# Kernel tuning notes

Measured on AMD Instinct MI355X. Metric: run time of the kernel, lower is better.

The kernel has to match this reference:

```python
import jax, jax.numpy as jnp
from jax import lax
import numpy as np

BN_EPS = 1e-3

def _hard_sigmoid(x):
    # Keras hard_sigmoid: relu6(x + 3) / 6
    return jnp.clip(x / 6.0 + 0.5, 0.0, 1.0)

def _conv(x, w):
    # x: [B,H,W,C], w: [kh,kw,C,Cout]
    return lax.conv_general_dilated(x, w, window_strides=(1, 1), padding='SAME',
                                    dimension_numbers=('NHWC', 'HWIO', 'NHWC'))

def _convlstm(x, Wx, Wh, b):
    # x: [B,T,H,W,C] -> [B,T,H,W,F]; gates packed i,f,c,o along last dim (Keras order)
    B, T, H, W, C = x.shape
    F = b.shape[0] // 4
    h0 = jnp.zeros((B, H, W, F), x.dtype)
    c0 = jnp.zeros_like(h0)

    def step(carry, xt):
        h, c = carry
        z = _conv(xt, Wx) + _conv(h, Wh) + b  # [B,H,W,4F]
        i, f, g, o = jnp.split(z, 4, axis=-1)
        c = _hard_sigmoid(f) * c + _hard_sigmoid(i) * jnp.tanh(g)
        h = _hard_sigmoid(o) * jnp.tanh(c)
        return (h, c), h

    _, hs = lax.scan(step, (h0, c0), jnp.moveaxis(x, 1, 0))  # [T,B,H,W,F]
    return jnp.moveaxis(hs, 0, 1)


def setup_inputs() -> dict:
    key = jax.random.key(0)
    ks = jax.random.split(key, 8)
    B, T, H, W, C, F = 4, 16, 64, 64, 48, 48
    x = jax.random.normal(ks[0], (B, T, H, W, C), jnp.float32)
    s = 0.05  # keep gate pre-activations in a sane range
    Wx1 = jax.random.normal(ks[1], (3, 3, C, 4 * F), jnp.float32) * s
    Wh1 = jax.random.normal(ks[2], (3, 3, F, 4 * F), jnp.float32) * s
    b1 = jax.random.normal(ks[3], (4 * F,), jnp.float32) * s
    Wx2 = jax.random.normal(ks[4], (3, 3, F, 4 * F), jnp.float32) * s
    Wh2 = jax.random.normal(ks[5], (3, 3, F, 4 * F), jnp.float32) * s
    b2 = jax.random.normal(ks[6], (4 * F,), jnp.float32) * s
    gamma = jnp.ones((F,), jnp.float32)
    beta = jnp.zeros((F,), jnp.float32)
    mean = jax.random.normal(ks[7], (F,), jnp.float32) * 0.1
    var = jax.random.uniform(jax.random.fold_in(key, 99), (F,), jnp.float32, 0.5, 1.5)
    return {"x": x, "Wx1": Wx1, "Wh1": Wh1, "b1": b1,
            "Wx2": Wx2, "Wh2": Wh2, "b2": b2,
            "gamma": gamma, "beta": beta, "mean": mean, "var": var}


def reference(x, Wx1, Wh1, b1, Wx2, Wh2, b2, gamma, beta, mean, var):
    h = _convlstm(x, Wx1, Wh1, b1)
    # Dropout(0.2) at inference: identity. BatchNorm (inference, per-channel):
    h = gamma * (h - mean) * lax.rsqrt(var + BN_EPS) + beta
    h = _convlstm(h, Wx2, Wh2, b2)
    return x + h  # channels match (C == filters) -> direct residual add
```

## Files before the change

### kernel.cpp

```cpp
#include <hip/hip_runtime.h>
#include <hip/hip_bf16.h>

typedef __bf16 bf16;
typedef __bf16 bf16x8 __attribute__((ext_vector_type(8)));
typedef float  f32x4  __attribute__((ext_vector_type(4)));
typedef unsigned short u16x8 __attribute__((ext_vector_type(8)));

#define NB 4
#define NT 16
#define NH 64
#define NW 64
#define NC 48
#define RSTR 104
#define RKY  (66*RSTR)

__device__ __forceinline__ float hsig(float x){
    return fminf(fmaxf(x*0.16666667f + 0.5f, 0.0f), 1.0f);
}
__device__ __forceinline__ float ftanh(float x){
    float ax = fabsf(x);
    float e  = __expf(-2.0f*ax);
    float r  = (1.0f - e) * __builtin_amdgcn_rcpf(1.0f + e);
    return __builtin_copysignf(r, x);
}

__global__ void detect_dtype(const unsigned* __restrict__ g, int* __restrict__ flag){
    if (threadIdx.x == 0 && blockIdx.x == 0)
        *flag = (g[0] == 0x3F803F80u) ? 1 : 0;
}

__device__ __forceinline__ float ld_any(const void* p, int i, int isbf){
    return isbf ? (float)((const bf16*)p)[i] : ((const float*)p)[i];
}

__global__ void prep_weights(const void* __restrict__ Wx, const void* __restrict__ Wh,
                             const int* __restrict__ flag, bf16* __restrict__ Wsw){
    int isbf = *flag;
    int idx = blockIdx.x*256 + threadIdx.x;
    if (idx >= 165888) return;
    int e    = idx & 7;
    int lane = (idx >> 3) & 63;
    int nt   = (idx >> 9) % 12;
    int krk  = idx / (512*12);
    int ky = krk / 9, kr = krk % 9;
    int ln = lane & 15, lg = lane >> 4;
    int n_new  = nt*16 + ln;
    int gate = n_new & 3, c = n_new >> 2;
    int n_orig = gate*48 + c;
    int k  = kr*32 + lg*8 + e;
    int kx = k / 96, ch = k % 96;
    float v = (ch < 48) ? ld_any(Wx, ((ky*3+kx)*48 + ch)*192 + n_orig, isbf)
                        : ld_any(Wh, ((ky*3+kx)*48 + (ch-48))*192 + n_orig, isbf);
    Wsw[idx] = (bf16)v;
}

__global__ void prep_params(const void* b1, const void* b2, const void* gamma,
                            const void* beta, const void* mean, const void* var,
                            const int* __restrict__ flag, float* __restrict__ P){
    int isbf = *flag;
    int i = blockIdx.x*64 + threadIdx.x;
    if (i < 192)      P[i] = ld_any(b1, i, isbf);
    else if (i < 384) P[i] = ld_any(b2, i-192, isbf);
    else if (i < 432){
        int c = i-384;
        P[i] = ld_any(gamma,c,isbf) * rsqrtf(ld_any(var,c,isbf) + 1e-3f);
    } else if (i < 480){
        int c = i-432;
        float sc = ld_any(gamma,c,isbf) * rsqrtf(ld_any(var,c,isbf) + 1e-3f);
        P[i] = ld_any(beta,c,isbf) - ld_any(mean,c,isbf)*sc;
    }
}

template<int LAYER>
__global__ __launch_bounds__(256, 1)
void step_kernel(const void* __restrict__ xseq,
                 const bf16* __restrict__ hin,
                 bf16*       __restrict__ hout,
                 float*      __restrict__ cbuf,
                 const bf16* __restrict__ Wsw,
                 const float* __restrict__ P,
                 const void* __restrict__ xres,
                 bf16*       __restrict__ seqout,
                 void*       __restrict__ outp,
                 const int* __restrict__ flag,
                 int t)
{
    __shared__ bf16  rowpad[3*RKY];
    __shared__ float zbuf[64*196];
    const int isbf = *flag;
    const int tid = threadIdx.x;
    const int img = blockIdx.x >> 6;
    const int y   = blockIdx.x & 63;

    if (tid < 78){
        int ky = tid/26; int rmd = tid%26;
        int col = (rmd < 13) ? 0 : 65; int q = rmd % 13;
        u16x8 z = {};
        *(u16x8*)(rowpad + ky*RKY + col*RSTR + q*8) = z;
    }
    for (int task = tid; task < 2304; task += 256){
        int part = task / 384;
        int chn  = task % 384;
        int ky = part >> 1, half = part & 1;
        int row = y + ky - 1;
        int xcol = chn / 6;
        int c0   = (chn % 6)*8;
        u16x8 val = {};
        if (row >= 0 && row < NH){
            if (half == 1){
                val = *(const u16x8*)(hin + ((img*NH + row)*NW + xcol)*NC + c0);
            } else {
                int si = (((img*NT + t)*NH + row)*NW + xcol)*NC + c0;
                if (LAYER == 2 || isbf){
                    val = *(const u16x8*)((const bf16*)xseq + si);
                } else {
                    const float* src = (const float*)xseq + si;
                    bf16x8 v;
                    #pragma unroll
                    for (int u = 0; u < 8; ++u) v[u] = (bf16)src[u];
                    val = *(u16x8*)&v;
                }
            }
        }
        *(u16x8*)(rowpad + ky*RKY + (xcol+1)*RSTR + half*48 + c0) = val;
    }
    __syncthreads();

    const int lane = tid & 63;
    const int wv   = tid >> 6;
    const int ln   = lane & 15;
    const int lg   = lane >> 4;

    f32x4 acc[4][3] = {};

    #pragma unroll
    for (int ky = 0; ky < 3; ++ky){
        #pragma unroll 3
        for (int kr = 0; kr < 9; ++kr){
            const bf16* wp = Wsw + (size_t)((ky*9 + kr)*12 + wv*3)*512 + lane*8;
            bf16x8 b0 = *(const bf16x8*)(wp);
            bf16x8 b1 = *(const bf16x8*)(wp + 512);
            bf16x8 b2 = *(const bf16x8*)(wp + 1024);
            const bf16* ap = rowpad + ky*RKY + (ln + (kr/3))*RSTR + (kr%3)*32 + lg*8;
            #pragma unroll
            for (int mt = 0; mt < 4; ++mt){
                bf16x8 a = *(const bf16x8*)(ap + mt*16*RSTR);
                acc[mt][0] = __builtin_amdgcn_mfma_f32_16x16x32_bf16(a, b0, acc[mt][0], 0,0,0);
                acc[mt][1] = __builtin_amdgcn_mfma_f32_16x16x32_bf16(a, b1, acc[mt][1], 0,0,0);
                acc[mt][2] = __builtin_amdgcn_mfma_f32_16x16x32_bf16(a, b2, acc[mt][2], 0,0,0);
            }
        }
    }

    #pragma unroll
    for (int mt = 0; mt < 4; ++mt)
        #pragma unroll
        for (int j = 0; j < 3; ++j)
            #pragma unroll
            for (int r = 0; r < 4; ++r)
                zbuf[(mt*16 + lg*4 + r)*196 + wv*48 + j*16 + ln] = acc[mt][j][r];
    __syncthreads();

    const float* Pb = P + (LAYER == 1 ? 0 : 192);
    #pragma unroll 4
    for (int it = 0; it < 12; ++it){
        int cell = tid + it*256;
        int pos  = cell / 48;
        int c    = cell - pos*48;
        f32x4 z = *(const f32x4*)(zbuf + pos*196 + c*4);
        float zi = z[0] + Pb[c];
        float zf = z[1] + Pb[48+c];
        float zg = z[2] + Pb[96+c];
        float zo = z[3] + Pb[144+c];
        int gi = ((img*NH + y)*NW + pos)*NC + c;
        float cold = cbuf[gi];
        float cn = hsig(zf)*cold + hsig(zi)*ftanh(zg);
        float hn = hsig(zo)*ftanh(cn);
        cbuf[gi] = cn;
        hout[gi] = (bf16)hn;
        int sidx = (((img*NT + t)*NH + y)*NW + pos)*NC + c;
        if (LAYER == 1){
            seqout[sidx] = (bf16)(hn*P[384+c] + P[432+c]);
        } else {
            float xr = isbf ? (float)((const bf16*)xres)[sidx]
                            : ((const float*)xres)[sidx];
            float v = xr + hn;
            if (isbf) ((bf16*)outp)[sidx] = (bf16)v;
            else      ((float*)outp)[sidx] = v;
        }
    }
}

extern "C" void kernel_launch(void* const* d_in, const int* in_sizes, int n_in,
                              void* d_out, int out_size, void* d_ws, size_t ws_size,
                              hipStream_t stream)
{
    const void* x     = d_in[0];
    const void* Wx1   = d_in[1];
    const void* Wh1   = d_in[2];
    const void* b1    = d_in[3];
    const void* Wx2   = d_in[4];
    const void* Wh2   = d_in[5];
    const void* b2    = d_in[6];
    const void* gamma = d_in[7];
    const void* beta  = d_in[8];
    const void* mean  = d_in[9];
    const void* var   = d_in[10];

    char* p = (char*)d_ws;
    auto carve = [&](size_t bytes)->void*{
        void* q = (void*)p; p += (bytes + 255) & ~(size_t)255; return q;
    };
    const size_t planeN = (size_t)NB*NH*NW*NC;
    int*   flag = (int*)  carve(256);
    float* P    = (float*)carve(480*sizeof(float));
    bf16*  Wc1  = (bf16*) carve(165888*sizeof(bf16));
    bf16*  Wc2  = (bf16*) carve(165888*sizeof(bf16));
    bf16*  hA   = (bf16*) carve(planeN*sizeof(bf16));
    bf16*  hB   = (bf16*) carve(planeN*sizeof(bf16));
    float* cb   = (float*)carve(planeN*sizeof(float));
    bf16*  seq  = (bf16*) carve((size_t)NB*NT*NH*NW*NC*sizeof(bf16));

    detect_dtype<<<1, 64, 0, stream>>>((const unsigned*)gamma, flag);

    prep_weights<<<648, 256, 0, stream>>>(Wx1, Wh1, flag, Wc1);
    prep_weights<<<648, 256, 0, stream>>>(Wx2, Wh2, flag, Wc2);
    prep_params<<<8, 64, 0, stream>>>(b1, b2, gamma, beta, mean, var, flag, P);

    hipMemsetAsync(hA, 0, planeN*sizeof(bf16),  stream);
    hipMemsetAsync(cb, 0, planeN*sizeof(float), stream);
    bf16 *hr = hA, *hw = hB;
    for (int t = 0; t < NT; ++t){
        step_kernel<1><<<NB*NH, 256, 0, stream>>>(x, hr, hw, cb, Wc1, P,
                                                  nullptr, seq, nullptr, flag, t);
        bf16* tmp = hr; hr = hw; hw = tmp;
    }
    hipMemsetAsync(hr, 0, planeN*sizeof(bf16),  stream);
    hipMemsetAsync(cb, 0, planeN*sizeof(float), stream);
    for (int t = 0; t < NT; ++t){
        step_kernel<2><<<NB*NH, 256, 0, stream>>>(seq, hr, hw, cb, Wc2, P,
                                                  x, nullptr, d_out, flag, t);
        bf16* tmp = hr; hr = hw; hw = tmp;
    }
}
```

Measured before the change: 685.1 us.

## Fuse all ConvLSTM timesteps and both layers into one persistent kernel

Replaces the 32 per-timestep launches with a single persistent kernel of 256 blocks, one per (image, row). Blocks synchronise through per-row progress flags, each waiting only on its two neighbouring rows, using release stores and spin-waits. The cell state stays in registers instead of a global buffer, and the block's own new h row goes straight into LDS. The next timestep's input rows are staged while the gates are computed, so launch overhead, the global cell-state traffic and memsets go away. The trade-off is that correctness depends on all blocks being resident at once (otherwise the spin-waits deadlock), and the cross-block flag protocol carries subtle race risks.

```diff
diff --git a/kernel.cpp b/kernel.cpp
--- a/kernel.cpp
+++ b/kernel.cpp
@@ -71,26 +71,33 @@
     }
 }
 
-template<int LAYER>
 __global__ __launch_bounds__(256, 1)
-void step_kernel(const void* __restrict__ xseq,
-                 const bf16* __restrict__ hin,
-                 bf16*       __restrict__ hout,
-                 float*      __restrict__ cbuf,
-                 const bf16* __restrict__ Wsw,
-                 const float* __restrict__ P,
-                 const void* __restrict__ xres,
-                 bf16*       __restrict__ seqout,
-                 void*       __restrict__ outp,
-                 const int* __restrict__ flag,
-                 int t)
+void fused_kernel(const void* __restrict__ x,
+                  bf16* __restrict__ seq,
+                  bf16* __restrict__ hA,
+                  bf16* __restrict__ hB,
+                  const bf16* __restrict__ Wc1,
+                  const bf16* __restrict__ Wc2,
+                  const float* __restrict__ P,
+                  void* __restrict__ outp,
+                  const int* __restrict__ flag,
+                  int* __restrict__ done)
 {
     __shared__ bf16  rowpad[3*RKY];
     __shared__ float zbuf[64*196];
     const int isbf = *flag;
-    const int tid = threadIdx.x;
-    const int img = blockIdx.x >> 6;
-    const int y   = blockIdx.x & 63;
+    const int tid  = threadIdx.x;
+    const int xcd  = blockIdx.x & 7;
+    const int slot = blockIdx.x >> 3;
+    const int img  = xcd >> 1;
+    const int y    = ((xcd & 1) << 5) | slot;
+    const int lane = tid & 63;
+    const int wv   = tid >> 6;
+    const int ln   = lane & 15;
+    const int lg   = lane >> 4;
+
+    int* dme  = done + img*NH + y;
+    int* dimg = done + img*NH;
 
     if (tid < 78){
         int ky = tid/26; int rmd = tid%26;
@@ -98,95 +105,150 @@
         u16x8 z = {};
         *(u16x8*)(rowpad + ky*RKY + col*RSTR + q*8) = z;
     }
-    for (int task = tid; task < 2304; task += 256){
-        int part = task / 384;
-        int chn  = task % 384;
-        int ky = part >> 1, half = part & 1;
-        int row = y + ky - 1;
-        int xcol = chn / 6;
-        int c0   = (chn % 6)*8;
-        u16x8 val = {};
-        if (row >= 0 && row < NH){
-            if (half == 1){
-                val = *(const u16x8*)(hin + ((img*NH + row)*NW + xcol)*NC + c0);
-            } else {
-                int si = (((img*NT + t)*NH + row)*NW + xcol)*NC + c0;
-                if (LAYER == 2 || isbf){
-                    val = *(const u16x8*)((const bf16*)xseq + si);
+
+    float creg[12];
+
+    #pragma unroll
+    for (int L = 0; L < 2; ++L){
+        const bf16*  Wsw = L ? Wc2 : Wc1;
+        const float* Pb  = P + (L ? 192 : 0);
+        const void*  xs  = L ? (const void*)seq : x;
+        const int    xbf = L ? 1 : isbf;
+
+        float bi_[3], bf_[3], bg_[3], bo_[3], bns[3], bnb[3];
+        #pragma unroll
+        for (int q = 0; q < 3; ++q){
+            int cq = (tid + q*16) % 48;
+            bi_[q] = Pb[cq];      bf_[q] = Pb[48+cq];
+            bg_[q] = Pb[96+cq];   bo_[q] = Pb[144+cq];
+            bns[q] = P[384+cq];   bnb[q] = P[432+cq];
+        }
+
+        auto stage_x = [&](int tt){
+            for (int task = tid; task < 1152; task += 256){
+                int ky = task/384, chn = task%384;
+                int xcol = chn/6, c0 = (chn%6)*8;
+                int row = y + ky - 1;
+                u16x8 val = {};
+                if (row >= 0 && row < NH){
+                    int si = (((img*NT + tt)*NH + row)*NW + xcol)*NC + c0;
+                    if (xbf){
+                        val = *(const u16x8*)((const bf16*)xs + si);
+                    } else {
+                        const float* src = (const float*)xs + si;
+                        bf16x8 v;
+                        #pragma unroll
+                        for (int u = 0; u < 8; ++u) v[u] = (bf16)src[u];
+                        val = *(u16x8*)&v;
+                    }
+                }
+                *(u16x8*)(rowpad + ky*RKY + (xcol+1)*RSTR + c0) = val;
+            }
+        };
+
+        stage_x(0);
+        for (int task = tid; task < 1152; task += 256){
+            int ky = task/384, chn = task%384;
+            int xcol = chn/6, c0 = (chn%6)*8;
+            u16x8 z = {};
+            *(u16x8*)(rowpad + ky*RKY + (xcol+1)*RSTR + 48 + c0) = z;
+        }
+        #pragma unroll
+        for (int i = 0; i < 12; ++i) creg[i] = 0.f;
+        __syncthreads();
+
+        #pragma unroll 1
+        for (int t = 0; t < NT; ++t){
+            bf16* hw = ((t + L) & 1) ? hB : hA;
+
+            f32x4 acc[4][3] = {};
+            #pragma unroll
+            for (int ky = 0; ky < 3; ++ky){
+                #pragma unroll 3
+                for (int kr = 0; kr < 9; ++kr){
+                    const bf16* wp = Wsw + (size_t)((ky*9 + kr)*12 + wv*3)*512 + lane*8;
+                    bf16x8 b0 = *(const bf16x8*)(wp);
+                    bf16x8 b1 = *(const bf16x8*)(wp + 512);
+                    bf16x8 b2 = *(const bf16x8*)(wp + 1024);
+                    const bf16* ap = rowpad + ky*RKY + (ln + (kr/3))*RSTR + (kr%3)*32 + lg*8;
+                    #pragma unroll
+                    for (int mt = 0; mt < 4; ++mt){
+                        bf16x8 a = *(const bf16x8*)(ap + mt*16*RSTR);
+                        acc[mt][0] = __builtin_amdgcn_mfma_f32_16x16x32_bf16(a, b0, acc[mt][0], 0,0,0);
+                        acc[mt][1] = __builtin_amdgcn_mfma_f32_16x16x32_bf16(a, b1, acc[mt][1], 0,0,0);
+                        acc[mt][2] = __builtin_amdgcn_mfma_f32_16x16x32_bf16(a, b2, acc[mt][2], 0,0,0);
+                    }
+                }
+            }
+
+            #pragma unroll
+            for (int mt = 0; mt < 4; ++mt)
+                #pragma unroll
+                for (int j = 0; j < 3; ++j)
+                    #pragma unroll
+                    for (int r = 0; r < 4; ++r)
+                        zbuf[(mt*16 + lg*4 + r)*196 + wv*48 + j*16 + ln] = acc[mt][j][r];
+            __syncthreads();
+
+            if (t < NT-1) stage_x(t+1);
+
+            #pragma unroll
+            for (int it = 0; it < 12; ++it){
+                const int q = it % 3;
+                int cell = tid + it*256;
+                int pos = cell/48;
+                int c = cell - pos*48;
+                f32x4 z = *(const f32x4*)(zbuf + pos*196 + c*4);
+                float cn = hsig(z[1]+bf_[q])*creg[it] + hsig(z[0]+bi_[q])*ftanh(z[2]+bg_[q]);
+                float hn = hsig(z[3]+bo_[q])*ftanh(cn);
+                creg[it] = cn;
+                if (t < NT-1){
+                    int gi = ((img*NH + y)*NW + pos)*NC + c;
+                    hw[gi] = (bf16)hn;
+                }
+                rowpad[RKY + (pos+1)*RSTR + 48 + c] = (bf16)hn;
+                int sidx = (((img*NT + t)*NH + y)*NW + pos)*NC + c;
+                if (L == 0){
+                    seq[sidx] = (bf16)(hn*bns[q] + bnb[q]);
                 } else {
-                    const float* src = (const float*)xseq + si;
-                    bf16x8 v;
-                    #pragma unroll
-                    for (int u = 0; u < 8; ++u) v[u] = (bf16)src[u];
-                    val = *(u16x8*)&v;
-                }
-            }
-        }
-        *(u16x8*)(rowpad + ky*RKY + (xcol+1)*RSTR + half*48 + c0) = val;
-    }
-    __syncthreads();
-
-    const int lane = tid & 63;
-    const int wv   = tid >> 6;
-    const int ln   = lane & 15;
-    const int lg   = lane >> 4;
-
-    f32x4 acc[4][3] = {};
-
-    #pragma unroll
-    for (int ky = 0; ky < 3; ++ky){
-        #pragma unroll 3
-        for (int kr = 0; kr < 9; ++kr){
-            const bf16* wp = Wsw + (size_t)((ky*9 + kr)*12 + wv*3)*512 + lane*8;
-            bf16x8 b0 = *(const bf16x8*)(wp);
-            bf16x8 b1 = *(const bf16x8*)(wp + 512);
-            bf16x8 b2 = *(const bf16x8*)(wp + 1024);
-            const bf16* ap = rowpad + ky*RKY + (ln + (kr/3))*RSTR + (kr%3)*32 + lg*8;
-            #pragma unroll
-            for (int mt = 0; mt < 4; ++mt){
-                bf16x8 a = *(const bf16x8*)(ap + mt*16*RSTR);
-                acc[mt][0] = __builtin_amdgcn_mfma_f32_16x16x32_bf16(a, b0, acc[mt][0], 0,0,0);
-                acc[mt][1] = __builtin_amdgcn_mfma_f32_16x16x32_bf16(a, b1, acc[mt][1], 0,0,0);
-                acc[mt][2] = __builtin_amdgcn_mfma_f32_16x16x32_bf16(a, b2, acc[mt][2], 0,0,0);
-            }
-        }
-    }
-
-    #pragma unroll
-    for (int mt = 0; mt < 4; ++mt)
-        #pragma unroll
-        for (int j = 0; j < 3; ++j)
-            #pragma unroll
-            for (int r = 0; r < 4; ++r)
-                zbuf[(mt*16 + lg*4 + r)*196 + wv*48 + j*16 + ln] = acc[mt][j][r];
-    __syncthreads();
-
-    const float* Pb = P + (LAYER == 1 ? 0 : 192);
-    #pragma unroll 4
-    for (int it = 0; it < 12; ++it){
-        int cell = tid + it*256;
-        int pos  = cell / 48;
-        int c    = cell - pos*48;
-        f32x4 z = *(const f32x4*)(zbuf + pos*196 + c*4);
-        float zi = z[0] + Pb[c];
-        float zf = z[1] + Pb[48+c];
-        float zg = z[2] + Pb[96+c];
-        float zo = z[3] + Pb[144+c];
-        int gi = ((img*NH + y)*NW + pos)*NC + c;
-        float cold = cbuf[gi];
-        float cn = hsig(zf)*cold + hsig(zi)*ftanh(zg);
-        float hn = hsig(zo)*ftanh(cn);
-        cbuf[gi] = cn;
-        hout[gi] = (bf16)hn;
-        int sidx = (((img*NT + t)*NH + y)*NW + pos)*NC + c;
-        if (LAYER == 1){
-            seqout[sidx] = (bf16)(hn*P[384+c] + P[432+c]);
-        } else {
-            float xr = isbf ? (float)((const bf16*)xres)[sidx]
-                            : ((const float*)xres)[sidx];
-            float v = xr + hn;
-            if (isbf) ((bf16*)outp)[sidx] = (bf16)v;
-            else      ((float*)outp)[sidx] = v;
+                    float xr = isbf ? (float)((const bf16*)x)[sidx]
+                                    : ((const float*)x)[sidx];
+                    float v = xr + hn;
+                    if (isbf) ((bf16*)outp)[sidx] = (bf16)v;
+                    else      ((float*)outp)[sidx] = v;
+                }
+            }
+
+            __syncthreads();
+            if (tid == 0)
+                __hip_atomic_store(dme, L*16 + t + 1,
+                                   __ATOMIC_RELEASE, __HIP_MEMORY_SCOPE_AGENT);
+
+            if (t < NT-1){
+                if (tid < 2){
+                    int nb = tid ? y+1 : y-1;
+                    if (nb >= 0 && nb < NH){
+                        const int need = L*16 + t + 1;
+                        while (__hip_atomic_load(dimg + nb, __ATOMIC_RELAXED,
+                                                 __HIP_MEMORY_SCOPE_AGENT) < need)
+                            __builtin_amdgcn_s_sleep(1);
+                    }
+                    __threadfence();
+                }
+                __syncthreads();
+                for (int task = tid; task < 768; task += 256){
+                    int kyh = task/384;
+                    int chn = task%384;
+                    int ky  = kyh << 1;
+                    int xcol = chn/6, c0 = (chn%6)*8;
+                    int row = y + ky - 1;
+                    u16x8 val = {};
+                    if (row >= 0 && row < NH)
+                        val = *(const u16x8*)(hw + ((img*NH + row)*NW + xcol)*NC + c0);
+                    *(u16x8*)(rowpad + ky*RKY + (xcol+1)*RSTR + 48 + c0) = val;
+                }
+                __syncthreads();
+            }
         }
     }
 }
@@ -218,28 +280,15 @@
     bf16*  Wc2  = (bf16*) carve(165888*sizeof(bf16));
     bf16*  hA   = (bf16*) carve(planeN*sizeof(bf16));
     bf16*  hB   = (bf16*) carve(planeN*sizeof(bf16));
-    float* cb   = (float*)carve(planeN*sizeof(float));
     bf16*  seq  = (bf16*) carve((size_t)NB*NT*NH*NW*NC*sizeof(bf16));
+    int*   done = (int*)  carve(NB*NH*sizeof(int));
 
     detect_dtype<<<1, 64, 0, stream>>>((const unsigned*)gamma, flag);
-
     prep_weights<<<648, 256, 0, stream>>>(Wx1, Wh1, flag, Wc1);
     prep_weights<<<648, 256, 0, stream>>>(Wx2, Wh2, flag, Wc2);
     prep_params<<<8, 64, 0, stream>>>(b1, b2, gamma, beta, mean, var, flag, P);
-
-    hipMemsetAsync(hA, 0, planeN*sizeof(bf16),  stream);
-    hipMemsetAsync(cb, 0, planeN*sizeof(float), stream);
-    bf16 *hr = hA, *hw = hB;
-    for (int t = 0; t < NT; ++t){
-        step_kernel<1><<<NB*NH, 256, 0, stream>>>(x, hr, hw, cb, Wc1, P,
-                                                  nullptr, seq, nullptr, flag, t);
-        bf16* tmp = hr; hr = hw; hw = tmp;
-    }
-    hipMemsetAsync(hr, 0, planeN*sizeof(bf16),  stream);
-    hipMemsetAsync(cb, 0, planeN*sizeof(float), stream);
-    for (int t = 0; t < NT; ++t){
-        step_kernel<2><<<NB*NH, 256, 0, stream>>>(seq, hr, hw, cb, Wc2, P,
-                                                  x, nullptr, d_out, flag, t);
-        bf16* tmp = hr; hr = hw; hw = tmp;
-    }
-}
+    hipMemsetAsync(done, 0, NB*NH*sizeof(int), stream);
+
+    fused_kernel<<<dim3(NB*NH), dim3(256), 0, stream>>>(
+        x, seq, hA, hB, Wc1, Wc2, P, d_out, flag, done);
+}
```

After: 807.6 us. 1.18x slower.
